# Kernel optimization log

Measured on AMD Instinct MI355X. Metric: run time of the kernel, lower is better.

The kernel has to match this reference:

```python
import jax, jax.numpy as jnp
import numpy as np

B, K, D, V = 4096, 128, 512, 128000


def setup_inputs() -> dict:
    key = jax.random.key(0)
    k1, k2, k3 = jax.random.split(key, 3)
    inp = jax.random.normal(k1, (B, D), dtype=jnp.float32)
    indices = jax.random.randint(k2, (B, K), 0, V, dtype=jnp.int64)
    # xavier_uniform: bound = sqrt(6/(fan_in+fan_out)) for weight [V, D]
    bound = float(np.sqrt(6.0 / (V + D)))
    weight = jax.random.uniform(k3, (V, D), dtype=jnp.float32, minval=-bound, maxval=bound)
    bias = jnp.zeros((V,), dtype=jnp.float32)
    return {"inp": inp, "indices": indices, "sparse": 1, "weight": weight, "bias": bias}


def reference(inp, indices, sparse, weight, bias):
    if sparse:
        # gather per-sample weight rows [B, K, D] and bias [B, K], then batched dot
        w = weight[indices]          # [B, K, D]
        b = bias[indices]            # [B, K]
        out = jnp.einsum('bkd,bd->bk', w, inp) + b
        return out
    else:
        return inp @ weight.T + bias
```

## Files before the change

### kernel.cpp

```cpp
#include <hip/hip_runtime.h>
#include <hip/hip_fp16.h>


constexpr int Bc = 4096;
constexpr int Kc = 128;
constexpr int Dc = 512;
constexpr int Vc = 128000;
constexpr int NB = Bc * Kc;

typedef float    f32x4 __attribute__((ext_vector_type(4)));
typedef unsigned u32x4 __attribute__((ext_vector_type(4)));

constexpr size_t WS_HIST   = 0;
constexpr size_t WS_CURSOR = 512000;
constexpr size_t WS_START  = 512256;
constexpr size_t WS_CUR    = 1024256;
constexpr size_t WS_PAIRS  = 1536256;
constexpr size_t WS_INPH   = WS_PAIRS + (size_t)NB * 4;
constexpr size_t WS_NEED   = WS_INPH + (size_t)Bc * Dc * 2;

__global__ __launch_bounds__(256) void hist_kernel(
    const int* __restrict__ indices, unsigned* __restrict__ hist)
{
    int i = blockIdx.x * 256 + threadIdx.x;
    if (i < NB) atomicAdd(&hist[indices[i]], 1u);
}

__global__ __launch_bounds__(256) void alloc_kernel(
    const unsigned* __restrict__ hist, unsigned* __restrict__ start,
    unsigned* __restrict__ cur, unsigned* __restrict__ cursor)
{
    int v = blockIdx.x * 256 + threadIdx.x;
    if (v < Vc) {
        unsigned c = hist[v];
        unsigned s = c ? atomicAdd(cursor, c) : 0u;
        start[v] = s;
        cur[v]   = s;
    }
}

__global__ __launch_bounds__(256) void scatter_kernel(
    const int* __restrict__ indices, unsigned* __restrict__ cur,
    unsigned* __restrict__ pairs)
{
    int i = blockIdx.x * 256 + threadIdx.x;
    if (i < NB) {
        unsigned pos = atomicAdd(&cur[indices[i]], 1u);
        pairs[pos] = (unsigned)i;
    }
}

__global__ __launch_bounds__(256) void convert_kernel(
    const float* __restrict__ inp, __half* __restrict__ inph)
{
    int i = blockIdx.x * 256 + threadIdx.x;
    float4 v = ((const float4*)inp)[i];
    union { __half2 h[2]; uint2 u; } cv;
    cv.h[0] = __floats2half2_rn(v.x, v.y);
    cv.h[1] = __floats2half2_rn(v.z, v.w);
    ((uint2*)inph)[i] = cv.u;
}

__device__ __forceinline__ float2 h2f(unsigned u) {
    union { unsigned u; __half2 h; } c; c.u = u;
    return __half22float2(c.h);
}

__device__ __forceinline__ float dot8(const f32x4& w0, const f32x4& w1, const u32x4& p) {
    float2 f0 = h2f(p.x), f1 = h2f(p.y), f2 = h2f(p.z), f3 = h2f(p.w);
    return w0.x * f0.x + w0.y * f0.y + w0.z * f1.x + w0.w * f1.y
         + w1.x * f2.x + w1.y * f2.y + w1.z * f3.x + w1.w * f3.y;
}

__global__ __launch_bounds__(256) void compute_kernel(
    const __half* __restrict__ inph,
    const float*  __restrict__ weight,
    const float*  __restrict__ bias,
    const unsigned* __restrict__ hist,
    const unsigned* __restrict__ start,
    const unsigned* __restrict__ pairs,
    float* __restrict__ out)
{
    const int wave = threadIdx.x >> 6;
    const int lane = threadIdx.x & 63;
    const int v    = blockIdx.x * 4 + wave;

    const unsigned cnt = __builtin_nontemporal_load(&hist[v]);
    if (cnt == 0) return;
    const unsigned st = __builtin_nontemporal_load(&start[v]);

    const f32x4* wrow = (const f32x4*)(weight + (size_t)v * Dc);
    const f32x4 w0 = __builtin_nontemporal_load(&wrow[2 * lane]);
    const f32x4 w1 = __builtin_nontemporal_load(&wrow[2 * lane + 1]);
    const float bv = __builtin_nontemporal_load(&bias[v]);

    unsigned e = 0;
    for (; e + 2 <= cnt; e += 2) {
        const unsigned i0 = __builtin_nontemporal_load(&pairs[st + e]);
        const unsigned i1 = __builtin_nontemporal_load(&pairs[st + e + 1]);
        const u32x4 p0 = ((const u32x4*)(inph + (size_t)(i0 >> 7) * Dc))[lane];
        const u32x4 p1 = ((const u32x4*)(inph + (size_t)(i1 >> 7) * Dc))[lane];
        float s0 = dot8(w0, w1, p0);
        float s1 = dot8(w0, w1, p1);
        #pragma unroll
        for (int off = 32; off > 0; off >>= 1) {
            s0 += __shfl_xor(s0, off, 64);
            s1 += __shfl_xor(s1, off, 64);
        }
        if (lane == 0) {
            __builtin_nontemporal_store(s0 + bv, &out[i0]);
            __builtin_nontemporal_store(s1 + bv, &out[i1]);
        }
    }
    if (e < cnt) {
        const unsigned i0 = __builtin_nontemporal_load(&pairs[st + e]);
        const u32x4 p0 = ((const u32x4*)(inph + (size_t)(i0 >> 7) * Dc))[lane];
        float s0 = dot8(w0, w1, p0);
        #pragma unroll
        for (int off = 32; off > 0; off >>= 1) s0 += __shfl_xor(s0, off, 64);
        if (lane == 0) __builtin_nontemporal_store(s0 + bv, &out[i0]);
    }
}

__global__ __launch_bounds__(256) void fallback_kernel(
    const float* __restrict__ inp, const int* __restrict__ indices,
    const float* __restrict__ weight, const float* __restrict__ bias,
    float* __restrict__ out)
{
    const int b = blockIdx.x, lane = threadIdx.x & 63, wave = threadIdx.x >> 6;
    const float4* inp_row = (const float4*)(inp + (size_t)b * Dc);
    const float4 a0 = inp_row[lane];
    const float4 a1 = inp_row[64 + lane];
    const int* idx_base = indices + (size_t)b * Kc;
    float* out_base = out + (size_t)b * Kc;
    #pragma unroll 4
    for (int i = 0; i < 32; ++i) {
        const int k = wave * 32 + i;
        const int idx = idx_base[k];
        const float4* wrow = (const float4*)(weight + (size_t)idx * Dc);
        const float4 w0 = wrow[lane];
        const float4 w1 = wrow[64 + lane];
        float s = a0.x * w0.x + a0.y * w0.y + a0.z * w0.z + a0.w * w0.w
                + a1.x * w1.x + a1.y * w1.y + a1.z * w1.z + a1.w * w1.w;
        #pragma unroll
        for (int off = 32; off > 0; off >>= 1) s += __shfl_xor(s, off, 64);
        if (lane == 0) out_base[k] = s + bias[idx];
    }
}

extern "C" void kernel_launch(void* const* d_in, const int* in_sizes, int n_in,
                              void* d_out, int out_size, void* d_ws, size_t ws_size,
                              hipStream_t stream) {
    const float* inp     = (const float*)d_in[0];
    const int*   indices = (const int*)  d_in[1];
    const float* weight  = (const float*)d_in[3];
    const float* bias    = (const float*)d_in[4];
    float*       out     = (float*)d_out;

    if (ws_size < WS_NEED) {
        fallback_kernel<<<Bc, 256, 0, stream>>>(inp, indices, weight, bias, out);
        return;
    }

    char* ws = (char*)d_ws;
    unsigned* hist   = (unsigned*)(ws + WS_HIST);
    unsigned* cursor = (unsigned*)(ws + WS_CURSOR);
    unsigned* start  = (unsigned*)(ws + WS_START);
    unsigned* cur    = (unsigned*)(ws + WS_CUR);
    unsigned* pairs  = (unsigned*)(ws + WS_PAIRS);
    __half*   inph   = (__half*)  (ws + WS_INPH);

    hipMemsetAsync(ws, 0, WS_START, stream);

    convert_kernel<<<(Bc * Dc / 4) / 256, 256, 0, stream>>>(inp, inph);
    hist_kernel   <<<(NB + 255) / 256, 256, 0, stream>>>(indices, hist);
    alloc_kernel  <<<(Vc + 255) / 256, 256, 0, stream>>>(hist, start, cur, cursor);
    scatter_kernel<<<(NB + 255) / 256, 256, 0, stream>>>(indices, cur, pairs);
    compute_kernel<<<Vc / 4,            256, 0, stream>>>(inph, weight, bias,
                                                          hist, start, pairs, out);
}
```

Before: 477.2 us.

## Split compute kernel into two passes over halves of the feature dimension

The compute kernel now runs twice, each pass covering half of D (256 elements). The first pass writes partial dot products to a workspace buffer and the second adds its half, the partial and the bias. The aim is to halve the fp16 input slice each pass touches, so the gathered activation working set (2 MB per half) fits in cache better. The cost is an extra kernel launch, a second pass over the pairs list and per-vocab metadata, extra partial writes and reads, and one extra global round trip per output.

Measured after the change: 551.6 us. 15.6% more time.

```diff
diff --git a/kernel.cpp b/kernel.cpp
--- a/kernel.cpp
+++ b/kernel.cpp
@@ -5,11 +5,12 @@
 constexpr int Bc = 4096;
 constexpr int Kc = 128;
 constexpr int Dc = 512;
+constexpr int Dh = 256;
 constexpr int Vc = 128000;
 constexpr int NB = Bc * Kc;
 
 typedef float    f32x4 __attribute__((ext_vector_type(4)));
-typedef unsigned u32x4 __attribute__((ext_vector_type(4)));
+typedef unsigned u32x2 __attribute__((ext_vector_type(2)));
 
 constexpr size_t WS_HIST   = 0;
 constexpr size_t WS_CURSOR = 512000;
@@ -17,7 +18,8 @@
 constexpr size_t WS_CUR    = 1024256;
 constexpr size_t WS_PAIRS  = 1536256;
 constexpr size_t WS_INPH   = WS_PAIRS + (size_t)NB * 4;
-constexpr size_t WS_NEED   = WS_INPH + (size_t)Bc * Dc * 2;
+constexpr size_t WS_PART   = WS_INPH + (size_t)Bc * Dc * 2;
+constexpr size_t WS_NEED   = WS_PART + (size_t)NB * 4;
 
 __global__ __launch_bounds__(256) void hist_kernel(
     const int* __restrict__ indices, unsigned* __restrict__ hist)
@@ -66,12 +68,12 @@
     return __half22float2(c.h);
 }
 
-__device__ __forceinline__ float dot8(const f32x4& w0, const f32x4& w1, const u32x4& p) {
-    float2 f0 = h2f(p.x), f1 = h2f(p.y), f2 = h2f(p.z), f3 = h2f(p.w);
-    return w0.x * f0.x + w0.y * f0.y + w0.z * f1.x + w0.w * f1.y
-         + w1.x * f2.x + w1.y * f2.y + w1.z * f3.x + w1.w * f3.y;
+__device__ __forceinline__ float dot4(const f32x4& w, const u32x2& p) {
+    float2 f0 = h2f(p.x), f1 = h2f(p.y);
+    return w.x * f0.x + w.y * f0.y + w.z * f1.x + w.w * f1.y;
 }
 
+template <int HALF>
 __global__ __launch_bounds__(256) void compute_kernel(
     const __half* __restrict__ inph,
     const float*  __restrict__ weight,
@@ -79,46 +81,54 @@
     const unsigned* __restrict__ hist,
     const unsigned* __restrict__ start,
     const unsigned* __restrict__ pairs,
+    float* __restrict__ part,
     float* __restrict__ out)
 {
     const int wave = threadIdx.x >> 6;
     const int lane = threadIdx.x & 63;
     const int v    = blockIdx.x * 4 + wave;
 
-    const unsigned cnt = __builtin_nontemporal_load(&hist[v]);
+    const unsigned cnt = hist[v];
     if (cnt == 0) return;
-    const unsigned st = __builtin_nontemporal_load(&start[v]);
+    const unsigned st = start[v];
 
-    const f32x4* wrow = (const f32x4*)(weight + (size_t)v * Dc);
-    const f32x4 w0 = __builtin_nontemporal_load(&wrow[2 * lane]);
-    const f32x4 w1 = __builtin_nontemporal_load(&wrow[2 * lane + 1]);
-    const float bv = __builtin_nontemporal_load(&bias[v]);
+    const f32x4* wbase = (const f32x4*)(weight + (size_t)v * Dc + HALF * Dh);
+    const f32x4 w = __builtin_nontemporal_load(&wbase[lane]);
+    const float bv = (HALF == 1) ? bias[v] : 0.0f;
 
     unsigned e = 0;
     for (; e + 2 <= cnt; e += 2) {
         const unsigned i0 = __builtin_nontemporal_load(&pairs[st + e]);
         const unsigned i1 = __builtin_nontemporal_load(&pairs[st + e + 1]);
-        const u32x4 p0 = ((const u32x4*)(inph + (size_t)(i0 >> 7) * Dc))[lane];
-        const u32x4 p1 = ((const u32x4*)(inph + (size_t)(i1 >> 7) * Dc))[lane];
-        float s0 = dot8(w0, w1, p0);
-        float s1 = dot8(w0, w1, p1);
+        const u32x2* r0 = (const u32x2*)(inph + (size_t)(i0 >> 7) * Dc + HALF * Dh);
+        const u32x2* r1 = (const u32x2*)(inph + (size_t)(i1 >> 7) * Dc + HALF * Dh);
+        float s0 = dot4(w, r0[lane]);
+        float s1 = dot4(w, r1[lane]);
         #pragma unroll
         for (int off = 32; off > 0; off >>= 1) {
             s0 += __shfl_xor(s0, off, 64);
             s1 += __shfl_xor(s1, off, 64);
         }
         if (lane == 0) {
-            __builtin_nontemporal_store(s0 + bv, &out[i0]);
-            __builtin_nontemporal_store(s1 + bv, &out[i1]);
+            if (HALF == 0) {
+                __builtin_nontemporal_store(s0, &part[i0]);
+                __builtin_nontemporal_store(s1, &part[i1]);
+            } else {
+                __builtin_nontemporal_store(part[i0] + s0 + bv, &out[i0]);
+                __builtin_nontemporal_store(part[i1] + s1 + bv, &out[i1]);
+            }
         }
     }
     if (e < cnt) {
         const unsigned i0 = __builtin_nontemporal_load(&pairs[st + e]);
-        const u32x4 p0 = ((const u32x4*)(inph + (size_t)(i0 >> 7) * Dc))[lane];
-        float s0 = dot8(w0, w1, p0);
+        const u32x2* r0 = (const u32x2*)(inph + (size_t)(i0 >> 7) * Dc + HALF * Dh);
+        float s0 = dot4(w, r0[lane]);
         #pragma unroll
         for (int off = 32; off > 0; off >>= 1) s0 += __shfl_xor(s0, off, 64);
-        if (lane == 0) __builtin_nontemporal_store(s0 + bv, &out[i0]);
+        if (lane == 0) {
+            if (HALF == 0) __builtin_nontemporal_store(s0, &part[i0]);
+            else           __builtin_nontemporal_store(part[i0] + s0 + bv, &out[i0]);
+        }
     }
 }
 
@@ -169,6 +179,7 @@
     unsigned* cur    = (unsigned*)(ws + WS_CUR);
     unsigned* pairs  = (unsigned*)(ws + WS_PAIRS);
     __half*   inph   = (__half*)  (ws + WS_INPH);
+    float*    part   = (float*)   (ws + WS_PART);
 
     hipMemsetAsync(ws, 0, WS_START, stream);
 
@@ -176,6 +187,8 @@
     hist_kernel   <<<(NB + 255) / 256, 256, 0, stream>>>(indices, hist);
     alloc_kernel  <<<(Vc + 255) / 256, 256, 0, stream>>>(hist, start, cur, cursor);
     scatter_kernel<<<(NB + 255) / 256, 256, 0, stream>>>(indices, cur, pairs);
-    compute_kernel<<<Vc / 4,            256, 0, stream>>>(inph, weight, bias,
-                                                          hist, start, pairs, out);
+    compute_kernel<0><<<Vc / 4, 256, 0, stream>>>(inph, weight, bias,
+                                                  hist, start, pairs, part, out);
+    compute_kernel<1><<<Vc / 4, 256, 0, stream>>>(inph, weight, bias,
+                                                  hist, start, pairs, part, out);
 }
```
